# Kernel tuning notes

Measured on AMD Instinct MI355X. Metric: run time of the kernel, lower is better.

The kernel has to match this reference:

```python
import jax, jax.numpy as jnp
import numpy as np

B, H, W = 16, 1024, 1024
BOUNDARY_WEIGHT = 2.0
FOCAL_ALPHA = 0.25
FOCAL_GAMMA = 2.0
SMOOTH = 1e-6


def setup_inputs() -> dict:
    key = jax.random.key(0)
    k1, k2, k3 = jax.random.split(key, 3)
    pred_masks = jax.random.normal(k1, (B, 1, H, W), dtype=jnp.float32)
    gt_masks = jax.random.bernoulli(k2, 0.5, (B, 1, H, W)).astype(jnp.float32)
    pred_iou = jax.random.uniform(k3, (B, 1), dtype=jnp.float32)
    return {"pred_masks": pred_masks, "gt_masks": gt_masks, "pred_iou": pred_iou}


def _bce_with_logits(x, t):
    # stable: softplus(x) - x*t == -[t*log(sig(x)) + (1-t)*log(1-sig(x))]
    return jax.nn.softplus(x) - x * t


def reference(pred_masks, gt_masks, pred_iou):
    x, t = pred_masks, gt_masks
    ce = _bce_with_logits(x, t)                      # (B,1,H,W)
    p = jax.nn.sigmoid(x)

    # focal loss
    p_t = p * t + (1.0 - p) * (1.0 - t)
    alpha_t = FOCAL_ALPHA * t + (1.0 - FOCAL_ALPHA) * (1.0 - t)
    focal = jnp.mean(alpha_t * ce * (1.0 - p_t) ** FOCAL_GAMMA)

    # dice loss
    intersection = jnp.sum(p * t, axis=(2, 3))       # (B,1)
    union = jnp.sum(p, axis=(2, 3)) + jnp.sum(t, axis=(2, 3))
    dice = 1.0 - jnp.mean((2.0 * intersection + SMOOTH) / (union + SMOOTH))

    # boundary-weighted BCE. In the source, dist = EDT(mask) is 0 at every
    # background pixel and dist_inv = EDT(1-mask) is 0 at every foreground
    # pixel, so min(dist, dist_inv) == 0 <= 3 at EVERY pixel -> the weight
    # map is uniformly boundary_weight. Faithful equivalent:
    boundary = BOUNDARY_WEIGHT * jnp.mean(ce)

    total = focal + dice + 0.5 * boundary

    # IoU auxiliary loss (thresholded prediction; no grad flows through >0.5)
    pred_bin = (p > 0.5).astype(x.dtype)
    inter = jnp.sum(pred_bin * t, axis=(1, 2, 3))    # (B,)
    uni = jnp.sum(pred_bin, axis=(1, 2, 3)) + jnp.sum(t, axis=(1, 2, 3)) - inter
    actual_iou = (inter + SMOOTH) / (uni + SMOOTH)
    iou_loss = jnp.mean((jnp.squeeze(pred_iou) - actual_iou) ** 2)

    return total + 0.1 * iou_loss
```

## Files before the change

kernel.cpp:

```cpp
#include <hip/hip_runtime.h>
#include <math.h>


#define HW_PIX (1024 * 1024)
#define BATCH 16
constexpr int THREADS = 256;
constexpr int PIX_PER_BLOCK = 2048;
constexpr int BLOCKS_PER_IMG = HW_PIX / PIX_PER_BLOCK;
constexpr int ITERS = PIX_PER_BLOCK / (THREADS * 4);

__global__ __launch_bounds__(THREADS, 8) void
loss_partial(const float* __restrict__ x, const float* __restrict__ t,
             float* __restrict__ acc) {
  const long base = (long)blockIdx.x * PIX_PER_BLOCK;
  const float4* __restrict__ x4 = (const float4*)(x + base);
  const float4* __restrict__ t4 = (const float4*)(t + base);

  float4 xv[ITERS], tv[ITERS];
#pragma unroll
  for (int i = 0; i < ITERS; ++i) {
    xv[i] = x4[threadIdx.x + i * THREADS];
    tv[i] = t4[threadIdx.x + i * THREADS];
  }
  __builtin_amdgcn_sched_barrier(0);

  float fsum = 0.f, csum = 0.f, isum = 0.f, psum = 0.f;
  unsigned tcnt = 0, bicnt = 0, bpcnt = 0;

#pragma unroll
  for (int i = 0; i < ITERS; ++i) {
    const float* xs = reinterpret_cast<const float*>(&xv[i]);
    const float* ts = reinterpret_cast<const float*>(&tv[i]);
#pragma unroll
    for (int j = 0; j < 4; ++j) {
      const float xx = xs[j];
      const float tt = ts[j];
      const float e = __expf(-fabsf(xx));
      const float s = 1.0f + e;
      const float r = __builtin_amdgcn_rcpf(s);
      const float p = (xx >= 0.0f) ? r : e * r;
      const float ce = fmaxf(xx, 0.0f) - xx * tt + __logf(s);
      const float om = fmaf(tt, 1.0f - 2.0f * p, p);
      const float at = 0.75f - 0.5f * tt;
      fsum += at * ce * om * om;
      csum += ce;
      isum = fmaf(p, tt, isum);
      psum += p;
      const unsigned long long mt = __ballot(tt != 0.0f);
      const unsigned long long mb = __ballot(xx > 0.0f);
      tcnt  += (unsigned)__popcll(mt);
      bpcnt += (unsigned)__popcll(mb);
      bicnt += (unsigned)__popcll(mt & mb);
    }
  }

  __shared__ float red[THREADS / 64][7];
  const int lane = threadIdx.x & 63;
  const int wave = threadIdx.x >> 6;
  float vals[4] = {fsum, csum, isum, psum};
#pragma unroll
  for (int k = 0; k < 4; ++k) {
    float v = vals[k];
#pragma unroll
    for (int off = 32; off > 0; off >>= 1) v += __shfl_down(v, off);
    if (lane == 0) red[wave][k] = v;
  }
  if (lane == 0) {
    red[wave][4] = (float)tcnt;
    red[wave][5] = (float)bicnt;
    red[wave][6] = (float)bpcnt;
  }
  __syncthreads();
  if (threadIdx.x < 7) {
    const int b = blockIdx.x / BLOCKS_PER_IMG;
    const float s = red[0][threadIdx.x] + red[1][threadIdx.x] +
                    red[2][threadIdx.x] + red[3][threadIdx.x];
    atomicAdd(&acc[b * 8 + threadIdx.x], s);
  }
}

__global__ void loss_final(const float* __restrict__ acc,
                           const float* __restrict__ pred_iou,
                           float* __restrict__ out) {
  constexpr float SMOOTH = 1e-6f;
  const int lane = threadIdx.x;
  float F = 0.f, C = 0.f, D = 0.f, Q = 0.f;
  if (lane < BATCH) {
    const float* a = acc + lane * 8;
    F = a[0];
    C = a[1];
    const float I = a[2], P = a[3], T = a[4], BI = a[5], BP = a[6];
    D = (2.0f * I + SMOOTH) / (P + T + SMOOTH);
    const float iou = (BI + SMOOTH) / (BP + T - BI + SMOOTH);
    const float d = pred_iou[lane] - iou;
    Q = d * d;
  }
#pragma unroll
  for (int off = 32; off > 0; off >>= 1) {
    F += __shfl_down(F, off);
    C += __shfl_down(C, off);
    D += __shfl_down(D, off);
    Q += __shfl_down(Q, off);
  }
  if (lane == 0) {
    const float invN = 1.0f / (float)((long)BATCH * HW_PIX);
    const float focal = F * invN;
    const float dice = 1.0f - D * (1.0f / (float)BATCH);
    const float half_boundary = C * invN;
    const float iou_loss = Q * (1.0f / (float)BATCH);
    out[0] = focal + dice + half_boundary + 0.1f * iou_loss;
  }
}

extern "C" void kernel_launch(void* const* d_in, const int* in_sizes, int n_in,
                              void* d_out, int out_size, void* d_ws,
                              size_t ws_size, hipStream_t stream) {
  const float* x = (const float*)d_in[0];
  const float* t = (const float*)d_in[1];
  const float* piou = (const float*)d_in[2];
  float* acc = (float*)d_ws;

  hipMemsetAsync(acc, 0, BATCH * 8 * sizeof(float), stream);
  loss_partial<<<BATCH * BLOCKS_PER_IMG, THREADS, 0, stream>>>(x, t, acc);
  loss_final<<<1, 64, 0, stream>>>(acc, piou, (float*)d_out);
}
```

Before: 161.2 us.

## Fuse final reduction via last-block ticket and stream chunks with prefetch

Cuts the grid from 8192 blocks to 2048, so each block now processes 8192 pixels as 8 chunks with a two-deep register prefetch pipeline. The separate finalize kernel is folded into the main kernel: a global ticket atomic picks the last block to finish, and that block computes the final loss. This removes one kernel launch and a quarter of the atomics, at the cost of a threadfence plus ticket atomic in every block and fewer blocks to hide latency.

```diff
diff --git a/kernel.cpp b/kernel.cpp
--- a/kernel.cpp
+++ b/kernel.cpp
@@ -5,59 +5,74 @@
 #define HW_PIX (1024 * 1024)
 #define BATCH 16
 constexpr int THREADS = 256;
-constexpr int PIX_PER_BLOCK = 2048;
-constexpr int BLOCKS_PER_IMG = HW_PIX / PIX_PER_BLOCK;
-constexpr int ITERS = PIX_PER_BLOCK / (THREADS * 4);
+constexpr int BLOCKS = 2048;
+constexpr int BLOCKS_PER_IMG = BLOCKS / BATCH;
+constexpr int PIX_PER_BLOCK = HW_PIX / BLOCKS_PER_IMG;
+constexpr int CHUNK_F4 = THREADS;
+constexpr int CHUNKS = PIX_PER_BLOCK / (CHUNK_F4 * 4);
+
+struct Accum {
+  float fsum, csum, isum, psum;
+  unsigned tcnt, bicnt, bpcnt;
+};
+
+__device__ __forceinline__ void process4(const float4 xv, const float4 tv,
+                                         Accum& a) {
+  const float* xs = reinterpret_cast<const float*>(&xv);
+  const float* ts = reinterpret_cast<const float*>(&tv);
+#pragma unroll
+  for (int j = 0; j < 4; ++j) {
+    const float xx = xs[j];
+    const float tt = ts[j];
+    const float e = __expf(-fabsf(xx));
+    const float s = 1.0f + e;
+    const float r = __builtin_amdgcn_rcpf(s);
+    const float p = (xx >= 0.0f) ? r : e * r;
+    const float ce = fmaxf(xx, 0.0f) - xx * tt + __logf(s);
+    const float om = fmaf(tt, 1.0f - 2.0f * p, p);
+    const float at = 0.75f - 0.5f * tt;
+    a.fsum += at * ce * om * om;
+    a.csum += ce;
+    a.isum = fmaf(p, tt, a.isum);
+    a.psum += p;
+    const unsigned long long mt = __ballot(tt != 0.0f);
+    const unsigned long long mb = __ballot(xx > 0.0f);
+    a.tcnt  += (unsigned)__popcll(mt);
+    a.bpcnt += (unsigned)__popcll(mb);
+    a.bicnt += (unsigned)__popcll(mt & mb);
+  }
+}
 
 __global__ __launch_bounds__(THREADS, 8) void
-loss_partial(const float* __restrict__ x, const float* __restrict__ t,
-             float* __restrict__ acc) {
+loss_fused(const float* __restrict__ x, const float* __restrict__ t,
+           const float* __restrict__ pred_iou, float* __restrict__ acc,
+           unsigned* __restrict__ ticket, float* __restrict__ out) {
+  const int b = blockIdx.x / BLOCKS_PER_IMG;
   const long base = (long)blockIdx.x * PIX_PER_BLOCK;
   const float4* __restrict__ x4 = (const float4*)(x + base);
   const float4* __restrict__ t4 = (const float4*)(t + base);
+  const int tid = threadIdx.x;
 
-  float4 xv[ITERS], tv[ITERS];
+  Accum a = {0.f, 0.f, 0.f, 0.f, 0u, 0u, 0u};
+
+  float4 xa = x4[tid + 0 * CHUNK_F4], ta = t4[tid + 0 * CHUNK_F4];
+  float4 xb = x4[tid + 1 * CHUNK_F4], tb = t4[tid + 1 * CHUNK_F4];
 #pragma unroll
-  for (int i = 0; i < ITERS; ++i) {
-    xv[i] = x4[threadIdx.x + i * THREADS];
-    tv[i] = t4[threadIdx.x + i * THREADS];
-  }
-  __builtin_amdgcn_sched_barrier(0);
-
-  float fsum = 0.f, csum = 0.f, isum = 0.f, psum = 0.f;
-  unsigned tcnt = 0, bicnt = 0, bpcnt = 0;
-
-#pragma unroll
-  for (int i = 0; i < ITERS; ++i) {
-    const float* xs = reinterpret_cast<const float*>(&xv[i]);
-    const float* ts = reinterpret_cast<const float*>(&tv[i]);
-#pragma unroll
-    for (int j = 0; j < 4; ++j) {
-      const float xx = xs[j];
-      const float tt = ts[j];
-      const float e = __expf(-fabsf(xx));
-      const float s = 1.0f + e;
-      const float r = __builtin_amdgcn_rcpf(s);
-      const float p = (xx >= 0.0f) ? r : e * r;
-      const float ce = fmaxf(xx, 0.0f) - xx * tt + __logf(s);
-      const float om = fmaf(tt, 1.0f - 2.0f * p, p);
-      const float at = 0.75f - 0.5f * tt;
-      fsum += at * ce * om * om;
-      csum += ce;
-      isum = fmaf(p, tt, isum);
-      psum += p;
-      const unsigned long long mt = __ballot(tt != 0.0f);
-      const unsigned long long mb = __ballot(xx > 0.0f);
-      tcnt  += (unsigned)__popcll(mt);
-      bpcnt += (unsigned)__popcll(mb);
-      bicnt += (unsigned)__popcll(mt & mb);
+  for (int c = 0; c < CHUNKS; ++c) {
+    float4 xn = xa, tn = ta;
+    if (c + 2 < CHUNKS) {
+      xn = x4[tid + (c + 2) * CHUNK_F4];
+      tn = t4[tid + (c + 2) * CHUNK_F4];
     }
+    process4(xa, ta, a);
+    xa = xb; ta = tb;
+    xb = xn; tb = tn;
   }
 
   __shared__ float red[THREADS / 64][7];
   const int lane = threadIdx.x & 63;
   const int wave = threadIdx.x >> 6;
-  float vals[4] = {fsum, csum, isum, psum};
+  float vals[4] = {a.fsum, a.csum, a.isum, a.psum};
 #pragma unroll
   for (int k = 0; k < 4; ++k) {
     float v = vals[k];
@@ -66,49 +81,52 @@
     if (lane == 0) red[wave][k] = v;
   }
   if (lane == 0) {
-    red[wave][4] = (float)tcnt;
-    red[wave][5] = (float)bicnt;
-    red[wave][6] = (float)bpcnt;
+    red[wave][4] = (float)a.tcnt;
+    red[wave][5] = (float)a.bicnt;
+    red[wave][6] = (float)a.bpcnt;
   }
   __syncthreads();
   if (threadIdx.x < 7) {
-    const int b = blockIdx.x / BLOCKS_PER_IMG;
     const float s = red[0][threadIdx.x] + red[1][threadIdx.x] +
                     red[2][threadIdx.x] + red[3][threadIdx.x];
     atomicAdd(&acc[b * 8 + threadIdx.x], s);
   }
-}
 
-__global__ void loss_final(const float* __restrict__ acc,
-                           const float* __restrict__ pred_iou,
-                           float* __restrict__ out) {
-  constexpr float SMOOTH = 1e-6f;
-  const int lane = threadIdx.x;
-  float F = 0.f, C = 0.f, D = 0.f, Q = 0.f;
-  if (lane < BATCH) {
-    const float* a = acc + lane * 8;
-    F = a[0];
-    C = a[1];
-    const float I = a[2], P = a[3], T = a[4], BI = a[5], BP = a[6];
-    D = (2.0f * I + SMOOTH) / (P + T + SMOOTH);
-    const float iou = (BI + SMOOTH) / (BP + T - BI + SMOOTH);
-    const float d = pred_iou[lane] - iou;
-    Q = d * d;
-  }
+  __shared__ unsigned is_last;
+  __threadfence();
+  __syncthreads();
+  if (threadIdx.x == 0)
+    is_last = (atomicAdd(ticket, 1u) == (unsigned)(BLOCKS - 1));
+  __syncthreads();
+  if (is_last && threadIdx.x < 64) {
+    __threadfence();
+    constexpr float SMOOTH = 1e-6f;
+    float F = 0.f, C = 0.f, D = 0.f, Q = 0.f;
+    if (lane < BATCH) {
+      const float* ap = acc + lane * 8;
+      F = ap[0];
+      C = ap[1];
+      const float I = ap[2], P = ap[3], T = ap[4], BI = ap[5], BP = ap[6];
+      D = (2.0f * I + SMOOTH) / (P + T + SMOOTH);
+      const float iou = (BI + SMOOTH) / (BP + T - BI + SMOOTH);
+      const float d = pred_iou[lane] - iou;
+      Q = d * d;
+    }
 #pragma unroll
-  for (int off = 32; off > 0; off >>= 1) {
-    F += __shfl_down(F, off);
-    C += __shfl_down(C, off);
-    D += __shfl_down(D, off);
-    Q += __shfl_down(Q, off);
-  }
-  if (lane == 0) {
-    const float invN = 1.0f / (float)((long)BATCH * HW_PIX);
-    const float focal = F * invN;
-    const float dice = 1.0f - D * (1.0f / (float)BATCH);
-    const float half_boundary = C * invN;
-    const float iou_loss = Q * (1.0f / (float)BATCH);
-    out[0] = focal + dice + half_boundary + 0.1f * iou_loss;
+    for (int off = 32; off > 0; off >>= 1) {
+      F += __shfl_down(F, off);
+      C += __shfl_down(C, off);
+      D += __shfl_down(D, off);
+      Q += __shfl_down(Q, off);
+    }
+    if (lane == 0) {
+      const float invN = 1.0f / (float)((long)BATCH * HW_PIX);
+      const float focal = F * invN;
+      const float dice = 1.0f - D * (1.0f / (float)BATCH);
+      const float half_boundary = C * invN;
+      const float iou_loss = Q * (1.0f / (float)BATCH);
+      out[0] = focal + dice + half_boundary + 0.1f * iou_loss;
+    }
   }
 }
 
@@ -119,8 +137,9 @@
   const float* t = (const float*)d_in[1];
   const float* piou = (const float*)d_in[2];
   float* acc = (float*)d_ws;
+  unsigned* ticket = (unsigned*)((char*)d_ws + 512);
 
-  hipMemsetAsync(acc, 0, BATCH * 8 * sizeof(float), stream);
-  loss_partial<<<BATCH * BLOCKS_PER_IMG, THREADS, 0, stream>>>(x, t, acc);
-  loss_final<<<1, 64, 0, stream>>>(acc, piou, (float*)d_out);
+  hipMemsetAsync(d_ws, 0, 640, stream);
+  loss_fused<<<BLOCKS, THREADS, 0, stream>>>(x, t, piou, acc, ticket,
+                                             (float*)d_out);
 }
```

After: 375.0 us. 2.33x slower.
